# Performance work log

Measured on AMD Instinct MI355X. Metric: run time of the kernel, lower is better.

Reference implementation:

```python
import jax, jax.numpy as jnp
import numpy as np

B, T, H = 256, 48, 512   # batch, timesteps, hidden (= size_seq feature dim)
S = H                    # size_seq == hidden feature dim (dim_seq_in = S+1)
K = 4                    # k_wk_ahead


def setup_inputs() -> dict:
    key = jax.random.key(0)
    ks = jax.random.split(key, 20)
    g = lambda k, shp: (jax.random.normal(k, shp, dtype=jnp.float32) * 0.05)
    inp = {
        "hiddens": jax.random.normal(ks[0], (B, T, S), dtype=jnp.float32),
        "allys": jax.random.normal(ks[1], (B, T), dtype=jnp.float32),
        "k_wk_ahead": K,
        # InputAttention params (Linear stored as [in, out])
        "Wh": g(ks[2], (H, S)), "bh": g(ks[3], (S,)),
        "Ws": g(ks[4], (S, S)), "bs": g(ks[5], (S,)),
        "Wo": g(ks[6], (S, 1)), "bo": g(ks[7], (1,)),
        # GRU params (torch layout: [3H, in]/[3H, H], gates ordered r,z,n)
        "W_ih": g(ks[8], (3 * H, S + 1)), "W_hh": g(ks[9], (3 * H, H)),
        "b_ih": g(ks[10], (3 * H,)), "b_hh": g(ks[11], (3 * H,)),
        # out_layer MLP: H->H/2->H/4->H/8->1 with LeakyReLU after each
        "W1": g(ks[12], (H, H // 2)), "b1": g(ks[13], (H // 2,)),
        "W2": g(ks[14], (H // 2, H // 4)), "b2": g(ks[15], (H // 4,)),
        "W3": g(ks[16], (H // 4, H // 8)), "b3": g(ks[17], (H // 8,)),
        "W4": g(ks[18], (H // 8, 1)), "b4": g(ks[19], (1,)),
    }
    return inp


def _gru_step(x, h, W_ih, W_hh, b_ih, b_hh):
    # torch GRU cell: gates ordered (reset, update, new)
    gi = x @ W_ih.T + b_ih          # [B, 3H]
    gh = h @ W_hh.T + b_hh          # [B, 3H]
    ir, iz, inn = jnp.split(gi, 3, axis=-1)
    hr, hz, hn = jnp.split(gh, 3, axis=-1)
    r = jax.nn.sigmoid(ir + hr)
    z = jax.nn.sigmoid(iz + hz)
    n = jnp.tanh(inn + r * hn)
    return (1.0 - z) * n + z * h


def reference(hiddens, allys, k_wk_ahead, Wh, bh, Ws, bs, Wo, bo,
              W_ih, W_hh, b_ih, b_hh, W1, b1, W2, b2, W3, b3, W4, b4):
    Bb, Tt, Ss = hiddens.shape
    # linearSignals(hiddens) is time-step-invariant: precompute once
    ls = hiddens @ Ws + bs                      # [B, T, S]

    def step(d_prev, ally_t):
        lh = d_prev @ Wh + bh                   # [B, S]
        e = jnp.tanh(lh[:, None, :] + ls) @ Wo + bo    # [B, T, 1]
        att = jax.nn.softmax(e, axis=1)[..., 0]        # [B, T]
        c = jnp.einsum('bt,bts->bs', att, hiddens)     # [B, S]
        x = jnp.concatenate([c, ally_t[:, None]], axis=1)   # [B, S+1]
        d = _gru_step(x, d_prev, W_ih, W_hh, b_ih, b_hh)
        return d, c

    d0 = jnp.zeros((Bb, W_hh.shape[1]), dtype=hiddens.dtype)
    d_last, cs = jax.lax.scan(step, d0, jnp.swapaxes(allys, 0, 1))
    c_last = cs[-1]                             # c_vectors[:, -1]

    def mlp(d):
        h = jax.nn.leaky_relu(d @ W1 + b1)
        h = jax.nn.leaky_relu(h @ W2 + b2)
        h = jax.nn.leaky_relu(h @ W3 + b3)
        return jax.nn.leaky_relu(h @ W4 + b4)   # dropout is identity in eval

    outs = []
    last_d = d_last
    for _ in range(k_wk_ahead):
        out = mlp(last_d)                       # [B, 1]
        outs.append(out)
        x = jnp.concatenate([c_last, out], axis=1)
        last_d = _gru_step(x, last_d, W_ih, W_hh, b_ih, b_hh)
    return jnp.stack(outs, axis=1)[..., 0]      # [B, K]
```

## Files before the change

kernel.cpp:

```cpp
#include <hip/hip_runtime.h>
#include <cstdio>

#ifndef __has_builtin
#define __has_builtin(x) 0
#endif

#define NB      256
#define NT      48
#define NS      512
#define KAHEAD  4
#define NTHREADS 1024
#define NBLOCKS  256
#define GSIZE    32
#define RSTRIDE  544
#define XSLOT    512
#define XROWB    1104

#define WS_D     0
#define WS_X     139264
#define WS_LH    278528
#define WS_BAR   409600
#define WS_WA    409856
#define WS_WC    934144
#define WS_WN    1196288
#define WS_WS    1327360
#define WS_FLOATS 1458432

#define L_XHI    0
#define L_XLO    35328
#define L_LSB    70656
#define L_GH     119808
#define L_GI     126336
#define L_LH     132864
#define L_WO     134912
#define L_E      136960
#define L_ATT    137216
#define L_H1P    139520
#define L_H1S    143616
#define L_H2P    144640
#define L_H2S    146688
#define L_H3P    147200
#define L_MISC   148224
#define L_PB     148240
#define LDS_BYTES 156432

typedef float    f4v  __attribute__((ext_vector_type(4)));
typedef float    f16v __attribute__((ext_vector_type(16)));
typedef _Float16 h4v  __attribute__((ext_vector_type(4)));
typedef _Float16 h8v  __attribute__((ext_vector_type(8)));

__device__ __forceinline__ f16v MFMA32(h8v a, h8v b, f16v c) {
    return __builtin_amdgcn_mfma_f32_32x32x16_f16(a, b, c, 0, 0, 0);
}
__device__ __forceinline__ f4v MFMA16(h8v a, h8v b, f4v c) {
    return __builtin_amdgcn_mfma_f32_16x16x32_f16(a, b, c, 0, 0, 0);
}

#if __has_builtin(__builtin_bit_cast)
#define F2H_BITS(v) __builtin_bit_cast(h8v, (v))
#define H2F_BITS(v) __builtin_bit_cast(f4v, (v))
#else
__device__ __forceinline__ h8v f2h_bits_(f4v v) { union { f4v f; h8v h; } u; u.f = v; return u.h; }
__device__ __forceinline__ f4v h2f_bits_(h8v v) { union { f4v f; h8v h; } u; u.h = v; return u.f; }
#define F2H_BITS(v) f2h_bits_(v)
#define H2F_BITS(v) h2f_bits_(v)
#endif

__device__ __forceinline__ float frcp_(float x) {
#if __has_builtin(__builtin_amdgcn_rcpf)
    return __builtin_amdgcn_rcpf(x);
#else
    return 1.0f / x;
#endif
}
__device__ __forceinline__ float ftanh_(float x) {
    float e = __expf(2.0f * x);
    return 1.0f - 2.0f * frcp_(e + 1.0f);
}
__device__ __forceinline__ float fsig_(float x) { return frcp_(1.0f + __expf(-x)); }
__device__ __forceinline__ float lrelu_(float x) { return fmaxf(x, 0.01f * x); }
__device__ __forceinline__ void split16_(float v, _Float16& hi, _Float16& lo) {
    _Float16 h = (_Float16)v;
    hi = h;
    lo = (_Float16)(v - (float)h);
}
__device__ __forceinline__ unsigned short f2hbits_(float v) {
    union { _Float16 h; unsigned short u; } c; c.h = (_Float16)v; return c.u;
}
__device__ __forceinline__ float hbits2f_(unsigned short u) {
    union { unsigned short u; _Float16 h; } c; c.u = u; return (float)c.h;
}

__device__ __forceinline__ void cstore1(float* p, float v) {
    asm volatile("global_store_dword %0, %1, off sc0" :: "v"(p), "v"(v) : "memory");
}
__device__ __forceinline__ f4v cload4(const float* p) {
    f4v v;
    asm volatile("global_load_dwordx4 %0, %1, off sc0" : "=v"(v) : "v"(p));
    return v;
}
__device__ __forceinline__ float cload1(const float* p) {
    float v;
    asm volatile("global_load_dword %0, %1, off sc0" : "=v"(v) : "v"(p));
    return v;
}
__device__ __forceinline__ void cwait() {
    asm volatile("s_waitcnt vmcnt(0)" ::: "memory");
    __builtin_amdgcn_sched_barrier(0);
}

__device__ __forceinline__ void gbar(unsigned* bar, unsigned* epoch) {
    asm volatile("s_waitcnt vmcnt(0)" ::: "memory");
    __syncthreads();
    if (threadIdx.x == 0) {
        *epoch += GSIZE;
        __hip_atomic_fetch_add(bar, 1u, __ATOMIC_RELAXED, __HIP_MEMORY_SCOPE_AGENT);
        unsigned target = *epoch;
        int guard = 0;
        while (__hip_atomic_load(bar, __ATOMIC_RELAXED, __HIP_MEMORY_SCOPE_AGENT) < target) {
#if __has_builtin(__builtin_amdgcn_s_sleep)
            __builtin_amdgcn_s_sleep(1);
#endif
            if (++guard > (1 << 17)) break;
        }
    }
    __syncthreads();
}

__device__ __forceinline__ void cvtStore_(char* hiB, char* loB, int idx, f4v v) {
    unsigned row = (unsigned)idx / 544u;
    unsigned col = (unsigned)idx - row * 544u;
    h4v h, l;
    #pragma unroll
    for (int i = 0; i < 4; ++i) { _Float16 hh, ll; split16_(v[i], hh, ll); h[i] = hh; l[i] = ll; }
    *(h4v*)(hiB + row * XROWB + col * 2) = h;
    *(h4v*)(loB + row * XROWB + col * 2) = l;
}
__device__ __forceinline__ void stagePanel(const float* __restrict__ gsrc,
                                           char* __restrict__ hiB,
                                           char* __restrict__ loB, int tid) {
    f4v v0 = cload4(gsrc + tid * 4);
    f4v v1 = cload4(gsrc + 4096 + tid * 4);
    f4v v2 = cload4(gsrc + 8192 + tid * 4);
    f4v v3 = cload4(gsrc + 12288 + tid * 4);
    f4v v4 = {0.f, 0.f, 0.f, 0.f};
    if (tid < 256) v4 = cload4(gsrc + 16384 + tid * 4);
    cwait();
    cvtStore_(hiB, loB, tid * 4, v0);
    cvtStore_(hiB, loB, 4096 + tid * 4, v1);
    cvtStore_(hiB, loB, 8192 + tid * 4, v2);
    cvtStore_(hiB, loB, 12288 + tid * 4, v3);
    if (tid < 256) cvtStore_(hiB, loB, 16384 + tid * 4, v4);
}

#define DO_GEMMA(doLH) do {                                                          \
    f16v acc_ = (f16v){0,0,0,0,0,0,0,0,0,0,0,0,0,0,0,0};                             \
    if (w < 4) {                                                                     \
        const int kc_ = w >> 1;                                                      \
        const int aoff_ = (l & 31) * XROWB + ((l >> 5) << 4);                        \
        _Pragma("unroll")                                                            \
        for (int kt = 0; kt < 16; ++kt) {                                            \
            h8v ah = *(const h8v*)(smem + L_XHI + aoff_ + (kc_ * 16 + kt) * 32);     \
            h8v al = *(const h8v*)(smem + L_XLO + aoff_ + (kc_ * 16 + kt) * 32);     \
            acc_ = MFMA32(ah, wreg[kt], acc_);                                       \
            acc_ = MFMA32(al, wreg[kt], acc_);                                       \
        }                                                                            \
        if (kc_ == 1) {                                                              \
            _Pragma("unroll")                                                        \
            for (int r = 0; r < 16; ++r) pbuf[(w & 1) * 1024 + r * 64 + l] = acc_[r];\
        }                                                                            \
    }                                                                                \
    __syncthreads();                                                                 \
    if (w < 2) {                                                                     \
        _Pragma("unroll")                                                            \
        for (int r = 0; r < 16; ++r) acc_[r] += pbuf[w * 1024 + r * 64 + l];         \
        const int c_ = w * 32 + (l & 31);                                            \
        const int rb_ = (l >> 5) << 2;                                               \
        if (c_ < 16) {                                                               \
            if (doLH) {                                                              \
                const int j_ = cix * 16 + c_;                                        \
                const float bb_ = bh[j_];                                            \
                _Pragma("unroll")                                                    \
                for (int r = 0; r < 16; ++r) {                                       \
                    int row_ = (r & 3) + ((r >> 2) << 3) + rb_;                      \
                    cstore1(lhw + (long)(g * 32 + row_) * NS + j_, acc_[r] + bb_);   \
                }                                                                    \
            }                                                                        \
        } else {                                                                     \
            const int gate_ = (c_ - 16) >> 4, jj_ = (c_ - 16) & 15;                  \
            const float bb_ = b_hh[gate_ * 512 + cix * 16 + jj_];                    \
            _Pragma("unroll")                                                        \
            for (int r = 0; r < 16; ++r) {                                           \
                int row_ = (r & 3) + ((r >> 2) << 3) + rb_;                          \
                ghs[gate_ * 544 + row_ * 17 + jj_] = acc_[r] + bb_;                  \
            }                                                                        \
        }                                                                            \
    }                                                                                \
} while (0)

#define DO_GEMMC() do {                                                              \
    f16v acc_ = (f16v){0,0,0,0,0,0,0,0,0,0,0,0,0,0,0,0};                             \
    f4v an0_ = {0.f,0.f,0.f,0.f}, an1_ = {0.f,0.f,0.f,0.f};                          \
    if (w == 4 || w == 5) {                                                          \
        const int kc_ = w - 4;                                                       \
        const int aoff_ = (l & 31) * XROWB + ((l >> 5) << 4);                        \
        _Pragma("unroll")                                                            \
        for (int kt = 0; kt < 16; ++kt) {                                            \
            h8v ah = *(const h8v*)(smem + L_XHI + aoff_ + (kc_ * 16 + kt) * 32);     \
            h8v al = *(const h8v*)(smem + L_XLO + aoff_ + (kc_ * 16 + kt) * 32);     \
            acc_ = MFMA32(ah, wreg[kt], acc_);                                       \
            acc_ = MFMA32(al, wreg[kt], acc_);                                       \
        }                                                                            \
        if (kc_ == 1) {                                                              \
            _Pragma("unroll")                                                        \
            for (int r = 0; r < 16; ++r) pbuf[r * 64 + l] = acc_[r];                 \
        }                                                                            \
    } else if (w == 6 || w == 7) {                                                   \
        const int kc_ = w - 6;                                                       \
        const int a0_ = (l & 15) * XROWB + ((l >> 4) << 4);                          \
        const int a1_ = a0_ + 16 * XROWB;                                            \
        _Pragma("unroll")                                                            \
        for (int kt = 0; kt < 8; ++kt) {                                             \
            const int kb_ = (kc_ * 8 + kt) * 64;                                     \
            h8v ah0 = *(const h8v*)(smem + L_XHI + a0_ + kb_);                       \
            h8v al0 = *(const h8v*)(smem + L_XLO + a0_ + kb_);                       \
            h8v ah1 = *(const h8v*)(smem + L_XHI + a1_ + kb_);                       \
            h8v al1 = *(const h8v*)(smem + L_XLO + a1_ + kb_);                       \
            an0_ = MFMA16(ah0, wreg[kt], an0_); an0_ = MFMA16(al0, wreg[kt], an0_);  \
            an1_ = MFMA16(ah1, wreg[kt], an1_); an1_ = MFMA16(al1, wreg[kt], an1_);  \
        }                                                                            \
        if (kc_ == 1) {                                                              \
            _Pragma("unroll")                                                        \
            for (int r = 0; r < 4; ++r) {                                            \
                pbuf[1024 + r * 64 + l] = an0_[r];                                   \
                pbuf[1280 + r * 64 + l] = an1_[r];                                   \
            }                                                                        \
        }                                                                            \
    }                                                                                \
    __syncthreads();                                                                 \
    if (w == 4) {                                                                    \
        _Pragma("unroll")                                                            \
        for (int r = 0; r < 16; ++r) acc_[r] += pbuf[r * 64 + l];                    \
        const int c_ = l & 31, gate_ = c_ >> 4, jj_ = c_ & 15;                       \
        const int rb_ = (l >> 5) << 2;                                               \
        const float bb_ = b_ih[gate_ * 512 + cix * 16 + jj_];                        \
        _Pragma("unroll")                                                            \
        for (int r = 0; r < 16; ++r) {                                               \
            int row_ = (r & 3) + ((r >> 2) << 3) + rb_;                              \
            gis[gate_ * 544 + row_ * 17 + jj_] = acc_[r] + bb_;                      \
        }                                                                            \
    } else if (w == 6) {                                                             \
        const int jj_ = l & 15;                                                      \
        const float bb_ = b_ih[1024 + cix * 16 + jj_];                               \
        _Pragma("unroll")                                                            \
        for (int r = 0; r < 4; ++r) {                                                \
            int row_ = ((l >> 4) << 2) + r;                                          \
            gis[1088 + row_ * 17 + jj_] = an0_[r] + pbuf[1024 + r * 64 + l] + bb_;   \
            gis[1088 + (16 + row_) * 17 + jj_] = an1_[r] + pbuf[1280 + r * 64 + l] + bb_; \
        }                                                                            \
    }                                                                                \
} while (0)

__device__ __forceinline__ void lsGemm(const char* smem, const _Float16* WS_,
        int tid, int ch, unsigned short* lsb, const float* bs) {
    const int w = tid >> 6, l = tid & 63;
    const int mt = w & 1, ng = w >> 1;
    const int aoff = (mt * 16 + (l & 15)) * XROWB + ((l >> 4) << 4);
    f4v acc[4] = {{0,0,0,0},{0,0,0,0},{0,0,0,0},{0,0,0,0}};
    for (int kt = 0; kt < 16; ++kt) {
        h8v ah = *(const h8v*)(smem + L_XHI + aoff + kt * 64);
        h8v al = *(const h8v*)(smem + L_XLO + aoff + kt * 64);
        #pragma unroll
        for (int i = 0; i < 4; ++i) {
            const _Float16* bp = WS_ + ((long)((ng * 4 + i) * 16 + kt)) * 512 + (l << 3);
            h8v bb = *(const h8v*)bp;
            acc[i] = MFMA16(ah, bb, acc[i]);
            acc[i] = MFMA16(al, bb, acc[i]);
        }
    }
    #pragma unroll
    for (int i = 0; i < 4; ++i) {
        const int n = (ng * 4 + i) * 16 + (l & 15);
        const float bsv = bs[n];
        #pragma unroll
        for (int r = 0; r < 4; ++r) {
            int row = mt * 16 + ((l >> 4) << 2) + r;
            if (row < 24)
                lsb[(ch * 24 + row) * NS + n] = f2hbits_(acc[i][r] + bsv);
        }
    }
}

__global__ void prep_kernel(const float* __restrict__ Whh,
                            const float* __restrict__ Wih,
                            const float* __restrict__ Wh,
                            const float* __restrict__ Ws,
                            float* __restrict__ ws) {
    long i = (long)blockIdx.x * blockDim.x + threadIdx.x;
    long stride = (long)gridDim.x * blockDim.x;
    _Float16* wa  = (_Float16*)(ws + WS_WA);
    _Float16* wc  = (_Float16*)(ws + WS_WC);
    _Float16* wn  = (_Float16*)(ws + WS_WN);
    _Float16* wsls = (_Float16*)(ws + WS_WS);

    for (long p = i; p < 131072; p += stride) {
        int l = (int)(p & 63);
        long t = p >> 6;
        int kt = (int)(t & 31);
        int u = (int)(t >> 5);
        int nt = u & 1, cix = u >> 1;
        int c = nt * 32 + (l & 31);
        #pragma unroll
        for (int e = 0; e < 8; ++e) {
            int k = kt * 16 + ((l >> 5) << 3) + e;
            float wv;
            if (c < 16) wv = Wh[(long)k * 512 + cix * 16 + c];
            else {
                int gate = (c - 16) >> 4, j = cix * 16 + ((c - 16) & 15);
                wv = Whh[((long)(gate * 512 + j)) * 512 + k];
            }
            wa[p * 8 + e] = (_Float16)wv;
        }
    }
    for (long p = i; p < 65536; p += stride) {
        int l = (int)(p & 63);
        long t = p >> 6;
        int kt = (int)(t & 31), cix = (int)(t >> 5);
        int c = l & 31, gate = c >> 4, j = cix * 16 + (c & 15);
        #pragma unroll
        for (int e = 0; e < 8; ++e) {
            int k = kt * 16 + ((l >> 5) << 3) + e;
            wc[p * 8 + e] = (_Float16)Wih[((long)(gate * 512 + j)) * 513 + k];
        }
    }
    for (long p = i; p < 32768; p += stride) {
        int l = (int)(p & 63);
        long t = p >> 6;
        int kt = (int)(t & 15), cix = (int)(t >> 4);
        int j = cix * 16 + (l & 15);
        #pragma unroll
        for (int e = 0; e < 8; ++e) {
            int k = kt * 32 + ((l >> 4) << 3) + e;
            wn[p * 8 + e] = (_Float16)Wih[((long)(1024 + j)) * 513 + k];
        }
    }
    for (long p = i; p < 32768; p += stride) {
        int l = (int)(p & 63);
        long t = p >> 6;
        int kt = (int)(t & 15), nt = (int)(t >> 4);
        int n = nt * 16 + (l & 15);
        #pragma unroll
        for (int e = 0; e < 8; ++e) {
            int k = kt * 32 + ((l >> 4) << 3) + e;
            wsls[p * 8 + e] = (_Float16)Ws[(long)k * 512 + n];
        }
    }
    for (long p = i; p < 278528; p += stride) ws[WS_D + p] = 0.0f;
    if (i < 256) ((unsigned*)(ws + WS_BAR))[i] = 0u;
}

__global__ void __launch_bounds__(NTHREADS, 4) fused_kernel(
        const float* __restrict__ hiddens, const float* __restrict__ allys,
        const float* __restrict__ bs,
        const float* __restrict__ Wo, const float* __restrict__ bo,
        const float* __restrict__ bh,
        const float* __restrict__ b_ih, const float* __restrict__ b_hh,
        const float* __restrict__ Wih,
        const float* __restrict__ W1, const float* __restrict__ b1,
        const float* __restrict__ W2, const float* __restrict__ b2,
        const float* __restrict__ W3, const float* __restrict__ b3,
        const float* __restrict__ W4, const float* __restrict__ b4,
        float* __restrict__ ws, float* __restrict__ out) {
    const int tid = threadIdx.x;

    float* dw  = ws + WS_D;
    float* xw  = ws + WS_X;
    float* lhw = ws + WS_LH;
    const _Float16* waF  = (const _Float16*)(ws + WS_WA);
    const _Float16* wcF  = (const _Float16*)(ws + WS_WC);
    const _Float16* wnF  = (const _Float16*)(ws + WS_WN);
    const _Float16* wsF  = (const _Float16*)(ws + WS_WS);
    unsigned* barbase = (unsigned*)(ws + WS_BAR);

    extern __shared__ char smem[];
    char*           xhi   = smem + L_XHI;
    char*           xlo   = smem + L_XLO;
    unsigned short* lsb   = (unsigned short*)(smem + L_LSB);
    float*          ghs   = (float*)(smem + L_GH);
    float*          gis   = (float*)(smem + L_GI);
    float*          lh_s  = (float*)(smem + L_LH);
    float*          wo_s  = (float*)(smem + L_WO);
    float*          e_s   = (float*)(smem + L_E);
    float*          att_s = (float*)(smem + L_ATT);
    float*          h1p   = (float*)(smem + L_H1P);
    float*          h1s   = (float*)(smem + L_H1S);
    float*          h2p   = (float*)(smem + L_H2P);
    float*          h2s   = (float*)(smem + L_H2S);
    float*          h3p   = (float*)(smem + L_H3P);
    int*            misc  = (int*)(smem + L_MISC);
    float*          pbuf  = (float*)(smem + L_PB);

    if (tid == 0) {
        unsigned xcc;
        asm volatile("s_getreg_b32 %0, hwreg(HW_REG_XCC_ID)" : "=s"(xcc));
        int gx = (int)(xcc & 7u);
        unsigned rk = __hip_atomic_fetch_add(barbase + gx * 32 + 1, 1u,
                                             __ATOMIC_RELAXED, __HIP_MEMORY_SCOPE_AGENT);
        misc[0] = gx;
        misc[1] = (int)(rk & 31u);
    }
    __syncthreads();
    const int g = misc[0], cix = misc[1];
    const int myb = g * 32 + cix;
    unsigned* bar = barbase + (g << 5);
    unsigned epoch = 0;

    const int w = tid >> 6, l = tid & 63;
    const int sS = tid & 511;
    const int rowE = tid >> 4, jE = tid & 15;
    const int jgE = cix * 16 + jE;
    const float* gPanelD = dw + (long)g * GSIZE * RSTRIDE;
    const float* gPanelX = xw + (long)g * GSIZE * RSTRIDE;

    float w512r = 0.f, w512z = 0.f, w512n = 0.f;
    if (tid < 512) {
        w512r = Wih[(long)jgE * 513 + 512];
        w512z = Wih[(long)(512 + jgE) * 513 + 512];
        w512n = Wih[(long)(1024 + jgE) * 513 + 512];
    }

    if (tid < NS) wo_s[tid] = Wo[tid];

    for (int i = tid; i < 4416; i += NTHREADS) *(f4v*)(smem + i * 16) = (f4v){0,0,0,0};
    for (int ch = 0; ch < 2; ++ch) {
        __syncthreads();
        {
            const float* src = hiddens + ((long)myb * NT + ch * 24) * NS;
            const int i0 = tid * 12;
            #pragma unroll
            for (int j3 = 0; j3 < 3; ++j3) {
                int idx = i0 + j3 * 4;
                f4v v = *(const f4v*)(src + idx);
                int row = idx >> 9, col = idx & 511;
                h4v h, lo;
                #pragma unroll
                for (int e = 0; e < 4; ++e) { _Float16 hh, ll; split16_(v[e], hh, ll); h[e] = hh; lo[e] = ll; }
                *(h4v*)(xhi + row * XROWB + col * 2) = h;
                *(h4v*)(xlo + row * XROWB + col * 2) = lo;
            }
        }
        __syncthreads();
        lsGemm(smem, wsF, tid, ch, lsb, bs);
    }
    __syncthreads();

    h8v wreg[16];
    if (w < 4) {
        const _Float16* p = waF + ((long)((cix * 2 + (w & 1)) * 32 + (w >> 1) * 16)) * 512 + (l << 3);
        #pragma unroll
        for (int kt = 0; kt < 16; ++kt) wreg[kt] = *(const h8v*)(p + kt * 512);
    } else if (w < 6) {
        const _Float16* p = wcF + ((long)(cix * 32 + (w - 4) * 16)) * 512 + (l << 3);
        #pragma unroll
        for (int kt = 0; kt < 16; ++kt) wreg[kt] = *(const h8v*)(p + kt * 512);
    } else if (w < 8) {
        const _Float16* p = wnF + ((long)(cix * 16 + (w - 6) * 8)) * 512 + (l << 3);
        #pragma unroll
        for (int kt = 0; kt < 8; ++kt) wreg[kt] = *(const h8v*)(p + kt * 512);
    } else {
        const float* hb = hiddens + (long)myb * NT * NS + sS;
        #pragma unroll
        for (int q = 0; q < 12; ++q) {
            f4v v = { hb[(q * 4 + 0) * 512], hb[(q * 4 + 1) * 512],
                      hb[(q * 4 + 2) * 512], hb[(q * 4 + 3) * 512] };
            wreg[q] = F2H_BITS(v);
        }
    }

    const float bo0 = bo[0];

    for (int t = 0; t < NT; ++t) {
        stagePanel(gPanelD, xhi, xlo, tid);
        __syncthreads();
        DO_GEMMA(true);
        gbar(bar, &epoch);

        if (tid < 128) {
            f4v v = cload4(lhw + (long)myb * NS + tid * 4);
            cwait();
            *(f4v*)(lh_s + tid * 4) = v;
        }
        if (tid == 0) cstore1(xw + (long)myb * RSTRIDE + XSLOT, allys[myb * NT + t]);
        __syncthreads();
        {
            const int wv = tid >> 6, ln = tid & 63;
            for (int q = 0; q < 3; ++q) {
                const int tt = wv * 3 + q;
                float p = 0.f;
                #pragma unroll
                for (int i2 = 0; i2 < 8; ++i2) {
                    int s = ln + (i2 << 6);
                    p = fmaf(wo_s[s], ftanh_(lh_s[s] + hbits2f_(lsb[tt * NS + s])), p);
                }
                #pragma unroll
                for (int off = 32; off >= 1; off >>= 1) p += __shfl_xor(p, off, 64);
                if (ln == 0) e_s[tt] = p + bo0;
            }
        }
        __syncthreads();
        if (tid < 64) {
            float v = (tid < NT) ? e_s[tid] : -1e30f;
            float m = v;
            #pragma unroll
            for (int off = 32; off >= 1; off >>= 1) m = fmaxf(m, __shfl_xor(m, off, 64));
            float ex = (tid < NT) ? __expf(v - m) : 0.0f;
            float ssum = ex;
            #pragma unroll
            for (int off = 32; off >= 1; off >>= 1) ssum += __shfl_xor(ssum, off, 64);
            if (tid < NT) att_s[tid] = ex * frcp_(ssum);
        }
        __syncthreads();
        if (tid >= 512) {
            float c = 0.f;
            #pragma unroll
            for (int q = 0; q < 12; ++q) {
                f4v hv = H2F_BITS(wreg[q]);
                c = fmaf(att_s[q * 4 + 0], hv.x, c);
                c = fmaf(att_s[q * 4 + 1], hv.y, c);
                c = fmaf(att_s[q * 4 + 2], hv.z, c);
                c = fmaf(att_s[q * 4 + 3], hv.w, c);
            }
            cstore1(xw + (long)myb * RSTRIDE + sS, c);
        }
        gbar(bar, &epoch);

        float hp = 0.f;
        if (tid < 512) hp = cload1(dw + (long)(g * 32 + rowE) * RSTRIDE + jgE);
        stagePanel(gPanelX, xhi, xlo, tid);
        __syncthreads();
        DO_GEMMC();
        __syncthreads();
        if (tid < 512) {
            float x512f = (float)*(const _Float16*)(xhi + rowE * XROWB + 1024)
                        + (float)*(const _Float16*)(xlo + rowE * XROWB + 1024);
            float gr  = fmaf(x512f, w512r, gis[rowE * 17 + jE]        + ghs[rowE * 17 + jE]);
            float gz  = fmaf(x512f, w512z, gis[544 + rowE * 17 + jE]  + ghs[544 + rowE * 17 + jE]);
            float gni = fmaf(x512f, w512n, gis[1088 + rowE * 17 + jE]);
            float gnh = ghs[1088 + rowE * 17 + jE];
            float rg = fsig_(gr);
            float zg = fsig_(gz);
            float ng = ftanh_(fmaf(rg, gnh, gni));
            cstore1(dw + (long)(g * 32 + rowE) * RSTRIDE + jgE, (1.f - zg) * ng + zg * hp);
        }
        gbar(bar, &epoch);
    }

    for (int kk = 0; kk < KAHEAD; ++kk) {
        {
            float v = 0.f;
            if (tid < NS) v = cload1(dw + (long)myb * RSTRIDE + tid);
            cwait();
            if (tid < NS) lh_s[tid] = v;
        }
        __syncthreads();
        {
            int n = tid & 255, q4 = tid >> 8;
            const float* av = lh_s + q4 * 128;
            const float* wp = W1 + (long)(q4 * 128) * 256 + n;
            float acc = 0.f;
            #pragma unroll 4
            for (int k2 = 0; k2 < 128; ++k2) { acc = fmaf(av[k2], wp[0], acc); wp += 256; }
            h1p[n * 4 + q4] = acc;
        }
        __syncthreads();
        if (tid < 256) {
            float v = h1p[tid * 4] + h1p[tid * 4 + 1] + h1p[tid * 4 + 2] + h1p[tid * 4 + 3];
            h1s[tid] = lrelu_(v + b1[tid]);
        }
        __syncthreads();
        if (tid < 512) {
            int n = tid & 127, q4 = tid >> 7;
            const float* av = h1s + q4 * 64;
            const float* wp = W2 + (long)(q4 * 64) * 128 + n;
            float acc = 0.f;
            #pragma unroll 4
            for (int k2 = 0; k2 < 64; ++k2) { acc = fmaf(av[k2], wp[0], acc); wp += 128; }
            h2p[n * 4 + q4] = acc;
        }
        __syncthreads();
        if (tid < 128) {
            float v = h2p[tid * 4] + h2p[tid * 4 + 1] + h2p[tid * 4 + 2] + h2p[tid * 4 + 3];
            h2s[tid] = lrelu_(v + b2[tid]);
        }
        __syncthreads();
        if (tid < 256) {
            int n = tid & 63, q4 = tid >> 6;
            const float* av = h2s + q4 * 32;
            const float* wp = W3 + (long)(q4 * 32) * 64 + n;
            float acc = 0.f;
            #pragma unroll 4
            for (int k2 = 0; k2 < 32; ++k2) { acc = fmaf(av[k2], wp[0], acc); wp += 64; }
            h3p[n * 4 + q4] = acc;
        }
        __syncthreads();
        if (tid < 64) {
            float v = h3p[tid * 4] + h3p[tid * 4 + 1] + h3p[tid * 4 + 2] + h3p[tid * 4 + 3];
            float h3v = lrelu_(v + b3[tid]);
            float p = h3v * W4[tid];
            #pragma unroll
            for (int off = 32; off >= 1; off >>= 1) p += __shfl_xor(p, off, 64);
            if (tid == 0) {
                float o = lrelu_(p + b4[0]);
                out[myb * KAHEAD + kk] = o;
                cstore1(xw + (long)myb * RSTRIDE + XSLOT, o);
            }
        }
        if (kk < KAHEAD - 1) {
            gbar(bar, &epoch);
            float hp = 0.f;
            if (tid < 512) hp = cload1(dw + (long)(g * 32 + rowE) * RSTRIDE + jgE);
            stagePanel(gPanelD, xhi, xlo, tid);
            __syncthreads();
            DO_GEMMA(false);
            __syncthreads();
            stagePanel(gPanelX, xhi, xlo, tid);
            __syncthreads();
            DO_GEMMC();
            __syncthreads();
            if (tid < 512) {
                float x512f = (float)*(const _Float16*)(xhi + rowE * XROWB + 1024)
                            + (float)*(const _Float16*)(xlo + rowE * XROWB + 1024);
                float gr  = fmaf(x512f, w512r, gis[rowE * 17 + jE]        + ghs[rowE * 17 + jE]);
                float gz  = fmaf(x512f, w512z, gis[544 + rowE * 17 + jE]  + ghs[544 + rowE * 17 + jE]);
                float gni = fmaf(x512f, w512n, gis[1088 + rowE * 17 + jE]);
                float gnh = ghs[1088 + rowE * 17 + jE];
                float rg = fsig_(gr);
                float zg = fsig_(gz);
                float ng = ftanh_(fmaf(rg, gnh, gni));
                cstore1(dw + (long)(g * 32 + rowE) * RSTRIDE + jgE, (1.f - zg) * ng + zg * hp);
            }
            gbar(bar, &epoch);
        }
    }
}

extern "C" void kernel_launch(void* const* d_in, const int* in_sizes, int n_in,
                              void* d_out, int out_size, void* d_ws, size_t ws_size,
                              hipStream_t stream) {
    const float* hiddens = (const float*)d_in[0];
    const float* allys   = (const float*)d_in[1];
    const float* Wh   = (const float*)d_in[3];
    const float* bh   = (const float*)d_in[4];
    const float* Ws   = (const float*)d_in[5];
    const float* bs   = (const float*)d_in[6];
    const float* Wo   = (const float*)d_in[7];
    const float* bo   = (const float*)d_in[8];
    const float* W_ih = (const float*)d_in[9];
    const float* W_hh = (const float*)d_in[10];
    const float* b_ih = (const float*)d_in[11];
    const float* b_hh = (const float*)d_in[12];
    const float* W1 = (const float*)d_in[13];
    const float* b1 = (const float*)d_in[14];
    const float* W2 = (const float*)d_in[15];
    const float* b2 = (const float*)d_in[16];
    const float* W3 = (const float*)d_in[17];
    const float* b3 = (const float*)d_in[18];
    const float* W4 = (const float*)d_in[19];
    const float* b4 = (const float*)d_in[20];
    float* wsf = (float*)d_ws;
    float* outf = (float*)d_out;

    if (ws_size < (size_t)WS_FLOATS * sizeof(float)) {
        fprintf(stderr, "kernel_launch: workspace too small (%zu < %zu)\n",
                ws_size, (size_t)WS_FLOATS * sizeof(float));
        return;
    }

    prep_kernel<<<dim3(2048), dim3(256), 0, stream>>>(W_hh, W_ih, Wh, Ws, wsf);

    (void)hipFuncSetAttribute((const void*)fused_kernel,
                              hipFuncAttributeMaxDynamicSharedMemorySize, LDS_BYTES);

    void* args[] = { &hiddens, &allys, &bs, &Wo, &bo, &bh,
                     &b_ih, &b_hh, &W_ih, &W1, &b1, &W2, &b2, &W3, &b3, &W4, &b4,
                     &wsf, &outf };
    hipError_t e = hipLaunchCooperativeKernel((void*)fused_kernel,
                                              dim3(NBLOCKS), dim3(NTHREADS),
                                              args, LDS_BYTES, stream);
    if (e != hipSuccess) {
        fprintf(stderr, "coop launch failed (%d); plain fallback\n", (int)e);
        (void)hipGetLastError();
        fused_kernel<<<dim3(NBLOCKS), dim3(NTHREADS), LDS_BYTES, stream>>>(
            hiddens, allys, bs, Wo, bo, bh, b_ih, b_hh, W_ih,
            W1, b1, W2, b2, W3, b3, W4, b4, wsf, outf);
    }
}
```

Before: 1.693 ms.

## Compute per-row attention projection locally to drop a grid barrier per step

Each block now computes its own batch row's d_prev@Wh+bh with extra waves (4-11) using MFMA on the staged panel and a new fp16 Wh layout prepared in the prep kernel. Previously each block computed a column slice for 32 rows and wrote it to global memory, which forced a grid-wide barrier and a global reload every timestep. Removing that barrier and round-trip shortens the serial per-step critical path. In exchange every block does redundant projection work (using only the hi part of the split fp16 input, so it loses some precision) and streams the full Wh matrix from cache each step.

```diff
diff --git a/kernel.cpp b/kernel.cpp
--- a/kernel.cpp
+++ b/kernel.cpp
@@ -18,7 +18,7 @@
 
 #define WS_D     0
 #define WS_X     139264
-#define WS_LH    278528
+#define WS_WHB   278528
 #define WS_BAR   409600
 #define WS_WA    409856
 #define WS_WC    934144
@@ -169,6 +169,21 @@
             _Pragma("unroll")                                                        \
             for (int r = 0; r < 16; ++r) pbuf[(w & 1) * 1024 + r * 64 + l] = acc_[r];\
         }                                                                            \
+    } else if (doLH && w < 12) {                                                     \
+        const int base_ = cix * XROWB + ((l >> 5) << 4);                             \
+        _Pragma("unroll")                                                            \
+        for (int sub_ = 0; sub_ < 2; ++sub_) {                                       \
+            const int nt_ = (w - 4) * 2 + sub_;                                      \
+            const _Float16* bp_ = whB + ((long)(nt_ * 32) << 9) + (l << 3);          \
+            f16v la_ = (f16v){0,0,0,0,0,0,0,0,0,0,0,0,0,0,0,0};                      \
+            _Pragma("unroll 8")                                                      \
+            for (int kt = 0; kt < 32; ++kt) {                                        \
+                h8v ah = *(const h8v*)(smem + L_XHI + base_ + kt * 32);              \
+                h8v bb = *(const h8v*)(bp_ + (kt << 9));                             \
+                la_ = MFMA32(ah, bb, la_);                                           \
+            }                                                                        \
+            if (l < 32) lh_s[nt_ * 32 + l] = la_[0] + bh[nt_ * 32 + l];              \
+        }                                                                            \
     }                                                                                \
     __syncthreads();                                                                 \
     if (w < 2) {                                                                     \
@@ -176,17 +191,7 @@
         for (int r = 0; r < 16; ++r) acc_[r] += pbuf[w * 1024 + r * 64 + l];         \
         const int c_ = w * 32 + (l & 31);                                            \
         const int rb_ = (l >> 5) << 2;                                               \
-        if (c_ < 16) {                                                               \
-            if (doLH) {                                                              \
-                const int j_ = cix * 16 + c_;                                        \
-                const float bb_ = bh[j_];                                            \
-                _Pragma("unroll")                                                    \
-                for (int r = 0; r < 16; ++r) {                                       \
-                    int row_ = (r & 3) + ((r >> 2) << 3) + rb_;                      \
-                    cstore1(lhw + (long)(g * 32 + row_) * NS + j_, acc_[r] + bb_);   \
-                }                                                                    \
-            }                                                                        \
-        } else {                                                                     \
+        if (c_ >= 16) {                                                              \
             const int gate_ = (c_ - 16) >> 4, jj_ = (c_ - 16) & 15;                  \
             const float bb_ = b_hh[gate_ * 512 + cix * 16 + jj_];                    \
             _Pragma("unroll")                                                        \
@@ -302,6 +307,7 @@
     _Float16* wc  = (_Float16*)(ws + WS_WC);
     _Float16* wn  = (_Float16*)(ws + WS_WN);
     _Float16* wsls = (_Float16*)(ws + WS_WS);
+    _Float16* whb = (_Float16*)(ws + WS_WHB);
 
     for (long p = i; p < 131072; p += stride) {
         int l = (int)(p & 63);
@@ -353,6 +359,17 @@
         for (int e = 0; e < 8; ++e) {
             int k = kt * 32 + ((l >> 4) << 3) + e;
             wsls[p * 8 + e] = (_Float16)Ws[(long)k * 512 + n];
+        }
+    }
+    for (long p = i; p < 32768; p += stride) {
+        int l = (int)(p & 63);
+        long t = p >> 6;
+        int kt = (int)(t & 31), nt = (int)(t >> 5);
+        int col = nt * 32 + (l & 31);
+        #pragma unroll
+        for (int e = 0; e < 8; ++e) {
+            int k = kt * 16 + ((l >> 5) << 3) + e;
+            whb[p * 8 + e] = (_Float16)Wh[(long)k * 512 + col];
         }
     }
     for (long p = i; p < 278528; p += stride) ws[WS_D + p] = 0.0f;
@@ -375,11 +392,11 @@
 
     float* dw  = ws + WS_D;
     float* xw  = ws + WS_X;
-    float* lhw = ws + WS_LH;
     const _Float16* waF  = (const _Float16*)(ws + WS_WA);
     const _Float16* wcF  = (const _Float16*)(ws + WS_WC);
     const _Float16* wnF  = (const _Float16*)(ws + WS_WN);
     const _Float16* wsF  = (const _Float16*)(ws + WS_WS);
+    const _Float16* whB  = (const _Float16*)(ws + WS_WHB);
     unsigned* barbase = (unsigned*)(ws + WS_BAR);
 
     extern __shared__ char smem[];
@@ -483,15 +500,7 @@
         stagePanel(gPanelD, xhi, xlo, tid);
         __syncthreads();
         DO_GEMMA(true);
-        gbar(bar, &epoch);
-
-        if (tid < 128) {
-            f4v v = cload4(lhw + (long)myb * NS + tid * 4);
-            cwait();
-            *(f4v*)(lh_s + tid * 4) = v;
-        }
         if (tid == 0) cstore1(xw + (long)myb * RSTRIDE + XSLOT, allys[myb * NT + t]);
-        __syncthreads();
         {
             const int wv = tid >> 6, ln = tid & 63;
             for (int q = 0; q < 3; ++q) {
```

New measurement: 2.072 ms. 1.22x slower.
